# Performance work log

Hardware: AMD Instinct MI355X
Metric: run time of the kernel (lower is better)

The kernel has to match this reference:

```python
import jax, jax.numpy as jnp
import numpy as np

EPS = 1e-8  # torch CosineSimilarity default eps

def _normalize(x):
    # torch clamps each norm at eps before dividing
    n = jnp.sqrt(jnp.sum(x * x, axis=-1, keepdims=True))
    return x / jnp.maximum(n, EPS)

def _cross_entropy(logits, labels):
    logp = jax.nn.log_softmax(logits, axis=-1)
    return -jnp.mean(jnp.take_along_axis(logp, labels[:, None], axis=-1))

def setup_inputs() -> dict:
    key = jax.random.key(0)
    ks = jax.random.split(key, 7)
    B, M, D = 8192, 3129, 512
    return {
        'mm_proj': jax.random.normal(ks[0], (B, D), jnp.float32),
        'ans_embedding': jax.random.normal(ks[1], (M, D), jnp.float32),
        'v_max': jax.random.normal(ks[2], (B, D), jnp.float32),
        'mm': jax.random.normal(ks[3], (B, D), jnp.float32),
        'logits_q': jax.random.normal(ks[4], (B, M), jnp.float32),
        'logits_rubi': jax.random.normal(ks[5], (B, M), jnp.float32),
        'class_id': jax.random.randint(ks[6], (B, 1), 0, M, jnp.int64),
    }

def reference(mm_proj, ans_embedding, v_max, mm, logits_q, logits_rubi, class_id,
              question_loss_weight=1.0):
    cid = class_id.squeeze(1)  # [B]
    # NCE over cosine similarities: fuse normalize + GEMM instead of [B,M,D] expand
    g = _normalize(mm_proj)          # [B, D]
    a = _normalize(ans_embedding)    # [M, D]
    d_logit = jnp.einsum('bd,md->bm', g, a)  # [B, M] cosine matrix
    positive_dist = jnp.take_along_axis(d_logit, cid[:, None], axis=1)[:, 0]  # [B]
    num = jnp.exp(positive_dist)
    den = jnp.sum(jnp.exp(d_logit), axis=-1)
    loss_nce = jnp.mean(-jnp.log(num / den))
    # object cosine loss
    obj_dist = jnp.sum(_normalize(v_max) * _normalize(mm), axis=-1)  # [B]
    obj_loss = jnp.mean(1.0 - obj_dist)
    fusion_loss = (_cross_entropy(logits_rubi, cid) + obj_loss + loss_nce) / 3.0
    question_loss = _cross_entropy(logits_q, cid)
    loss = fusion_loss + question_loss_weight * question_loss
    # out['loss'], out['loss_mm_q'], out['loss_q']
    return jnp.stack([loss, fusion_loss, question_loss])
```

## Files before the change

kernel.cpp:

```cpp
#include <hip/hip_runtime.h>
#include <hip/hip_bf16.h>

#define B_N 8192
#define M_N 3129
#define M_PAD 3200
#define D_N 512

#define GLOBAL_AS __attribute__((address_space(1)))
#define LDS_AS __attribute__((address_space(3)))

typedef __bf16 bf16x8 __attribute__((ext_vector_type(8)));
typedef float f32x4 __attribute__((ext_vector_type(4)));

#define PREP_G_BLOCKS   (B_N / 4)
#define PREP_A_BLOCKS   (M_PAD / 4)
#define PREP_OBJ_BLOCKS (B_N / 4)

__device__ __forceinline__ void normalize_row(
    const float* __restrict__ x, __bf16* __restrict__ y,
    int row, int nrows_src, int lane) {
  bf16x8 out;
  if (row >= nrows_src) {
    for (int j = 0; j < 8; ++j) out[j] = (__bf16)0.0f;
    *(bf16x8*)(y + (size_t)row * D_N + lane * 8) = out;
    return;
  }
  const float4* xr = (const float4*)(x + (size_t)row * D_N);
  float4 v0 = xr[lane * 2], v1 = xr[lane * 2 + 1];
  float s = v0.x*v0.x + v0.y*v0.y + v0.z*v0.z + v0.w*v0.w
          + v1.x*v1.x + v1.y*v1.y + v1.z*v1.z + v1.w*v1.w;
  for (int o = 1; o < 64; o <<= 1) s += __shfl_xor(s, o);
  float rn = 1.0f / fmaxf(sqrtf(s), 1e-8f);
  float vals[8] = {v0.x, v0.y, v0.z, v0.w, v1.x, v1.y, v1.z, v1.w};
  for (int j = 0; j < 8; ++j) out[j] = (__bf16)(vals[j] * rn);
  *(bf16x8*)(y + (size_t)row * D_N + lane * 8) = out;
}

__global__ __launch_bounds__(256) void prep_kernel(
    const float* __restrict__ mm_proj, const float* __restrict__ ans_emb,
    const float* __restrict__ v_max, const float* __restrict__ mm,
    __bf16* __restrict__ g, __bf16* __restrict__ a,
    float* __restrict__ obj) {
  int blk = blockIdx.x;
  int wid = threadIdx.x >> 6, lane = threadIdx.x & 63;
  if (blk < PREP_G_BLOCKS) {
    normalize_row(mm_proj, g, blk * 4 + wid, B_N, lane);
  } else if (blk < PREP_G_BLOCKS + PREP_A_BLOCKS) {
    normalize_row(ans_emb, a, (blk - PREP_G_BLOCKS) * 4 + wid, M_N, lane);
  } else {
    int b = (blk - PREP_G_BLOCKS - PREP_A_BLOCKS) * 4 + wid;
    const float4* vr = (const float4*)(v_max + (size_t)b * D_N);
    const float4* mr = (const float4*)(mm + (size_t)b * D_N);
    float4 a0 = vr[lane * 2], a1 = vr[lane * 2 + 1];
    float4 b0 = mr[lane * 2], b1 = mr[lane * 2 + 1];
    float sv = a0.x*a0.x + a0.y*a0.y + a0.z*a0.z + a0.w*a0.w
             + a1.x*a1.x + a1.y*a1.y + a1.z*a1.z + a1.w*a1.w;
    float sm = b0.x*b0.x + b0.y*b0.y + b0.z*b0.z + b0.w*b0.w
             + b1.x*b1.x + b1.y*b1.y + b1.z*b1.z + b1.w*b1.w;
    float sd = a0.x*b0.x + a0.y*b0.y + a0.z*b0.z + a0.w*b0.w
             + a1.x*b1.x + a1.y*b1.y + a1.z*b1.z + a1.w*b1.w;
    for (int o = 1; o < 64; o <<= 1) {
      sv += __shfl_xor(sv, o);
      sm += __shfl_xor(sm, o);
      sd += __shfl_xor(sd, o);
    }
    if (lane == 0) {
      float dist = sd / (fmaxf(sqrtf(sv), 1e-8f) * fmaxf(sqrtf(sm), 1e-8f));
      obj[b] = 1.0f - dist;
    }
  }
}

__global__ __launch_bounds__(256) void pos_kernel(
    const __bf16* __restrict__ g, const __bf16* __restrict__ a,
    const int* __restrict__ cid, float* __restrict__ pos) {
  int wid = threadIdx.x >> 6, lane = threadIdx.x & 63;
  int b = blockIdx.x * 4 + wid;
  if (b >= B_N) return;
  int label = cid[b];
  bf16x8 gv = *(const bf16x8*)(g + (size_t)b * D_N + lane * 8);
  bf16x8 av = *(const bf16x8*)(a + (size_t)label * D_N + lane * 8);
  float s = 0.0f;
  for (int j = 0; j < 8; ++j) s += (float)gv[j] * (float)av[j];
  for (int o = 1; o < 64; o <<= 1) s += __shfl_xor(s, o);
  if (lane == 0) pos[b] = s;
}

__global__ __launch_bounds__(256) void nce_gemm_kernel(
    const __bf16* __restrict__ g, const __bf16* __restrict__ a,
    float* __restrict__ den) {
  __shared__ __bf16 As[128 * 32];
  __shared__ __bf16 Bs[128 * 32];
  const int t = threadIdx.x;
  const int brow0 = blockIdx.y * 128;
  const int mrow0 = blockIdx.x * 128;
  const int lane = t & 63;
  const int wid = t >> 6;
  const int wrow = wid >> 1;
  const int wcol = wid & 1;
  const int r = lane & 15;
  const int quad = lane >> 4;

  f32x4 acc[4][4];
  for (int i = 0; i < 4; ++i)
    for (int j = 0; j < 4; ++j)
      acc[i][j] = f32x4{0.f, 0.f, 0.f, 0.f};

  for (int k0 = 0; k0 < D_N; k0 += 32) {
    __syncthreads();
    for (int i = 0; i < 2; ++i) {
      int s = t + i * 256;
      int row = s >> 2;
      int kq = (s & 3) << 3;
      const __bf16* ga = g + (size_t)(brow0 + row) * D_N + (k0 + kq);
      __builtin_amdgcn_global_load_lds((const GLOBAL_AS void*)ga,
                                       (LDS_AS void*)(As + s * 8), 16, 0, 0);
      const __bf16* gb = a + (size_t)(mrow0 + row) * D_N + (k0 + kq);
      __builtin_amdgcn_global_load_lds((const GLOBAL_AS void*)gb,
                                       (LDS_AS void*)(Bs + s * 8), 16, 0, 0);
    }
    __syncthreads();
    bf16x8 af[4], bf[4];
    for (int i = 0; i < 4; ++i)
      af[i] = *(const bf16x8*)(As + (wrow * 64 + i * 16 + r) * 32 + quad * 8);
    for (int j = 0; j < 4; ++j)
      bf[j] = *(const bf16x8*)(Bs + (wcol * 64 + j * 16 + r) * 32 + quad * 8);
    for (int i = 0; i < 4; ++i)
      for (int j = 0; j < 4; ++j)
        acc[i][j] = __builtin_amdgcn_mfma_f32_16x16x32_bf16(af[i], bf[j],
                                                            acc[i][j], 0, 0, 0);
  }

  for (int i = 0; i < 4; ++i) {
    for (int reg = 0; reg < 4; ++reg) {
      float s = 0.0f;
      for (int j = 0; j < 4; ++j) {
        int m = mrow0 + wcol * 64 + j * 16 + r;
        if (m < M_N) s += __expf(acc[i][j][reg]);
      }
      s += __shfl_xor(s, 1);
      s += __shfl_xor(s, 2);
      s += __shfl_xor(s, 4);
      s += __shfl_xor(s, 8);
      if (r == 0) {
        int b = brow0 + wrow * 64 + i * 16 + quad * 4 + reg;
        atomicAdd(den + b, s);
      }
    }
  }
}

#define CE_CHUNKS 784

__global__ __launch_bounds__(256) void ce_kernel(
    const float* __restrict__ lq, const float* __restrict__ lr,
    const int* __restrict__ cid,
    float* __restrict__ ce_q, float* __restrict__ ce_r) {
  __shared__ float Lq[CE_CHUNKS * 4];
  __shared__ float Lr[CE_CHUNKS * 4];
  const int b = blockIdx.x;
  const int t = threadIdx.x;
  const size_t start = ((size_t)b * M_N) & ~(size_t)3;
  const int mis = b & 3;
  const size_t TOTAL = (size_t)B_N * M_N;

#pragma unroll
  for (int k = 0; k < 3; ++k) {
    int c = t + k * 256;
    size_t gi = start + (size_t)c * 4;
    if (gi + 4 > TOTAL) gi = TOTAL - 4;
    __builtin_amdgcn_global_load_lds((const GLOBAL_AS void*)(lq + gi),
                                     (LDS_AS void*)(Lq + c * 4), 16, 0, 0);
    __builtin_amdgcn_global_load_lds((const GLOBAL_AS void*)(lr + gi),
                                     (LDS_AS void*)(Lr + c * 4), 16, 0, 0);
  }
  if (t < CE_CHUNKS - 768) {
    int c = t + 768;
    size_t gi = start + (size_t)c * 4;
    if (gi + 4 > TOTAL) gi = TOTAL - 4;
    __builtin_amdgcn_global_load_lds((const GLOBAL_AS void*)(lq + gi),
                                     (LDS_AS void*)(Lq + c * 4), 16, 0, 0);
    __builtin_amdgcn_global_load_lds((const GLOBAL_AS void*)(lr + gi),
                                     (LDS_AS void*)(Lr + c * 4), 16, 0, 0);
  }
  __syncthreads();

  const int lo = mis, hi = mis + M_N;
  float sq = 0.0f, sr = 0.0f;
#pragma unroll
  for (int k = 0; k < 4; ++k) {
    int c = t + k * 256;
    if (c < CE_CHUNKS) {
      float4 q = *(const float4*)(Lq + c * 4);
      float4 p = *(const float4*)(Lr + c * 4);
      int e = c * 4;
      if (e + 0 >= lo && e + 0 < hi) { sq += __expf(q.x); sr += __expf(p.x); }
      if (e + 1 >= lo && e + 1 < hi) { sq += __expf(q.y); sr += __expf(p.y); }
      if (e + 2 >= lo && e + 2 < hi) { sq += __expf(q.z); sr += __expf(p.z); }
      if (e + 3 >= lo && e + 3 < hi) { sq += __expf(q.w); sr += __expf(p.w); }
    }
  }
  for (int o = 1; o < 64; o <<= 1) {
    sq += __shfl_xor(sq, o);
    sr += __shfl_xor(sr, o);
  }
  __shared__ float ssq[4], ssr[4];
  int wid = t >> 6;
  if ((t & 63) == 0) { ssq[wid] = sq; ssr[wid] = sr; }
  __syncthreads();
  if (t == 0) {
    float tq = ssq[0] + ssq[1] + ssq[2] + ssq[3];
    float tr = ssr[0] + ssr[1] + ssr[2] + ssr[3];
    int label = cid[b];
    ce_q[b] = logf(tq) - Lq[mis + label];
    ce_r[b] = logf(tr) - Lr[mis + label];
  }
}

__global__ __launch_bounds__(256) void final_reduce_kernel(
    const float* __restrict__ den, const float* __restrict__ pos,
    const float* __restrict__ ce_q, const float* __restrict__ ce_r,
    const float* __restrict__ obj, float* __restrict__ acc) {
  int b = blockIdx.x * 256 + threadIdx.x;
  float s_nce = logf(den[b]) - pos[b];
  float s_ceq = ce_q[b];
  float s_cer = ce_r[b];
  float s_obj = obj[b];
  for (int o = 1; o < 64; o <<= 1) {
    s_nce += __shfl_xor(s_nce, o);
    s_ceq += __shfl_xor(s_ceq, o);
    s_cer += __shfl_xor(s_cer, o);
    s_obj += __shfl_xor(s_obj, o);
  }
  __shared__ float red[4][4];
  int wid = threadIdx.x >> 6;
  if ((threadIdx.x & 63) == 0) {
    red[wid][0] = s_nce; red[wid][1] = s_ceq;
    red[wid][2] = s_cer; red[wid][3] = s_obj;
  }
  __syncthreads();
  if (threadIdx.x < 4) {
    float v = red[0][threadIdx.x] + red[1][threadIdx.x]
            + red[2][threadIdx.x] + red[3][threadIdx.x];
    atomicAdd(acc + threadIdx.x, v);
  }
}

__global__ void final_combine_kernel(const float* __restrict__ acc,
                                     float* __restrict__ out) {
  if (threadIdx.x == 0) {
    float nce = acc[0] / (float)B_N;
    float ceq = acc[1] / (float)B_N;
    float cer = acc[2] / (float)B_N;
    float ob  = acc[3] / (float)B_N;
    float fusion = (cer + ob + nce) * (1.0f / 3.0f);
    out[0] = fusion + ceq;
    out[1] = fusion;
    out[2] = ceq;
  }
}

extern "C" void kernel_launch(void* const* d_in, const int* in_sizes, int n_in,
                              void* d_out, int out_size, void* d_ws, size_t ws_size,
                              hipStream_t stream) {
  const float* mm_proj     = (const float*)d_in[0];
  const float* ans_emb     = (const float*)d_in[1];
  const float* v_max       = (const float*)d_in[2];
  const float* mm          = (const float*)d_in[3];
  const float* logits_q    = (const float*)d_in[4];
  const float* logits_rubi = (const float*)d_in[5];
  const int*   cid         = (const int*)d_in[6];
  float* out = (float*)d_out;

  char* ws = (char*)d_ws;
  __bf16* g = (__bf16*)ws;
  __bf16* a = (__bf16*)(ws + 8388608);
  float* den  = (float*)(ws + 8388608 + 3276800);
  float* acc  = den + B_N;
  float* pos  = acc + 4;
  float* ce_q = pos + B_N;
  float* ce_r = ce_q + B_N;
  float* obj  = ce_r + B_N;

  hipMemsetAsync(den, 0, (size_t)(B_N + 4) * sizeof(float), stream);

  prep_kernel<<<PREP_G_BLOCKS + PREP_A_BLOCKS + PREP_OBJ_BLOCKS, 256, 0,
                stream>>>(mm_proj, ans_emb, v_max, mm, g, a, obj);
  pos_kernel<<<B_N / 4, 256, 0, stream>>>(g, a, cid, pos);
  nce_gemm_kernel<<<dim3(M_PAD / 128, B_N / 128), 256, 0, stream>>>(g, a, den);
  ce_kernel<<<B_N, 256, 0, stream>>>(logits_q, logits_rubi, cid, ce_q, ce_r);
  final_reduce_kernel<<<B_N / 256, 256, 0, stream>>>(den, pos, ce_q, ce_r,
                                                     obj, acc);
  final_combine_kernel<<<1, 64, 0, stream>>>(acc, out);
}
```

Measured before the change: 325.1 us.

## Flatten cross-entropy row sums into grid-stride wave chunks with atomic row accumulation

Replaces the per-row CE kernel, which staged each 3129-float row into LDS, with a flat streaming kernel. Each wave reads contiguous 1 KB chunks of both logits arrays directly into registers, splits each chunk's exp-sum between at most two rows, and atomically adds into per-row sums. The label logit gather and the log move into the final reduce kernel. This aims for fully coalesced aligned loads and no LDS round-trip or block syncs, at the cost of many atomics and a longer memset.

```diff
diff --git a/kernel.cpp b/kernel.cpp
--- a/kernel.cpp
+++ b/kernel.cpp
@@ -5,6 +5,11 @@
 #define M_N 3129
 #define M_PAD 3200
 #define D_N 512
+
+#define CE_WPA 100128
+#define CE_WTOT (2 * CE_WPA)
+#define CE_WAVES 8344
+#define CE_BLOCKS 2086
 
 #define GLOBAL_AS __attribute__((address_space(1)))
 #define LDS_AS __attribute__((address_space(3)))
@@ -150,81 +155,66 @@
   }
 }
 
-#define CE_CHUNKS 784
-
-__global__ __launch_bounds__(256) void ce_kernel(
+__global__ __launch_bounds__(256) void ce_sum_kernel(
     const float* __restrict__ lq, const float* __restrict__ lr,
-    const int* __restrict__ cid,
-    float* __restrict__ ce_q, float* __restrict__ ce_r) {
-  __shared__ float Lq[CE_CHUNKS * 4];
-  __shared__ float Lr[CE_CHUNKS * 4];
-  const int b = blockIdx.x;
-  const int t = threadIdx.x;
-  const size_t start = ((size_t)b * M_N) & ~(size_t)3;
-  const int mis = b & 3;
-  const size_t TOTAL = (size_t)B_N * M_N;
-
+    float* __restrict__ rowsum) {
+  const int lane = threadIdx.x & 63;
+  const int gw = (int)((blockIdx.x * 256 + threadIdx.x) >> 6);
+#pragma unroll 1
+  for (int gidx = 0; gidx < 6; ++gidx) {
+    float4 v[4];
+    unsigned e0[4];
+    int arr[4];
 #pragma unroll
-  for (int k = 0; k < 3; ++k) {
-    int c = t + k * 256;
-    size_t gi = start + (size_t)c * 4;
-    if (gi + 4 > TOTAL) gi = TOTAL - 4;
-    __builtin_amdgcn_global_load_lds((const GLOBAL_AS void*)(lq + gi),
-                                     (LDS_AS void*)(Lq + c * 4), 16, 0, 0);
-    __builtin_amdgcn_global_load_lds((const GLOBAL_AS void*)(lr + gi),
-                                     (LDS_AS void*)(Lr + c * 4), 16, 0, 0);
-  }
-  if (t < CE_CHUNKS - 768) {
-    int c = t + 768;
-    size_t gi = start + (size_t)c * 4;
-    if (gi + 4 > TOTAL) gi = TOTAL - 4;
-    __builtin_amdgcn_global_load_lds((const GLOBAL_AS void*)(lq + gi),
-                                     (LDS_AS void*)(Lq + c * 4), 16, 0, 0);
-    __builtin_amdgcn_global_load_lds((const GLOBAL_AS void*)(lr + gi),
-                                     (LDS_AS void*)(Lr + c * 4), 16, 0, 0);
-  }
-  __syncthreads();
-
-  const int lo = mis, hi = mis + M_N;
-  float sq = 0.0f, sr = 0.0f;
+    for (int k = 0; k < 4; ++k) {
+      int w = gw + (gidx * 4 + k) * CE_WAVES;
+      int aidx = (w >= CE_WPA) ? 1 : 0;
+      unsigned chunk = (unsigned)(w - aidx * CE_WPA) * 64u + (unsigned)lane;
+      e0[k] = chunk * 4u;
+      arr[k] = aidx;
+      const float* base = aidx ? lr : lq;
+      v[k] = *(const float4*)(base + (size_t)chunk * 4u);
+    }
 #pragma unroll
-  for (int k = 0; k < 4; ++k) {
-    int c = t + k * 256;
-    if (c < CE_CHUNKS) {
-      float4 q = *(const float4*)(Lq + c * 4);
-      float4 p = *(const float4*)(Lr + c * 4);
-      int e = c * 4;
-      if (e + 0 >= lo && e + 0 < hi) { sq += __expf(q.x); sr += __expf(p.x); }
-      if (e + 1 >= lo && e + 1 < hi) { sq += __expf(q.y); sr += __expf(p.y); }
-      if (e + 2 >= lo && e + 2 < hi) { sq += __expf(q.z); sr += __expf(p.z); }
-      if (e + 3 >= lo && e + 3 < hi) { sq += __expf(q.w); sr += __expf(p.w); }
-    }
-  }
-  for (int o = 1; o < 64; o <<= 1) {
-    sq += __shfl_xor(sq, o);
-    sr += __shfl_xor(sr, o);
-  }
-  __shared__ float ssq[4], ssr[4];
-  int wid = t >> 6;
-  if ((t & 63) == 0) { ssq[wid] = sq; ssr[wid] = sr; }
-  __syncthreads();
-  if (t == 0) {
-    float tq = ssq[0] + ssq[1] + ssq[2] + ssq[3];
-    float tr = ssr[0] + ssr[1] + ssr[2] + ssr[3];
-    int label = cid[b];
-    ce_q[b] = logf(tq) - Lq[mis + label];
-    ce_r[b] = logf(tr) - Lr[mis + label];
+    for (int k = 0; k < 4; ++k) {
+      unsigned row0 = e0[k] / M_N;
+      unsigned bound = (row0 + 1u) * M_N;
+      float ex0 = __expf(v[k].x), ex1 = __expf(v[k].y),
+            ex2 = __expf(v[k].z), ex3 = __expf(v[k].w);
+      float s_lo = 0.f, s_hi = 0.f;
+      if (e0[k] + 0u < bound) s_lo += ex0; else s_hi += ex0;
+      if (e0[k] + 1u < bound) s_lo += ex1; else s_hi += ex1;
+      if (e0[k] + 2u < bound) s_lo += ex2; else s_hi += ex2;
+      if (e0[k] + 3u < bound) s_lo += ex3; else s_hi += ex3;
+      unsigned rA = (unsigned)__builtin_amdgcn_readfirstlane((int)row0);
+      float cA = (row0 == rA) ? s_lo : 0.f;
+      float cB = (row0 == rA) ? s_hi : s_lo;
+      for (int o = 1; o < 64; o <<= 1) {
+        cA += __shfl_xor(cA, o);
+        cB += __shfl_xor(cB, o);
+      }
+      if (lane == 0) {
+        float* rs = rowsum + (arr[k] ? B_N : 0);
+        atomicAdd(rs + rA, cA);
+        if (cB != 0.f) atomicAdd(rs + rA + 1, cB);
+      }
+    }
   }
 }
 
 __global__ __launch_bounds__(256) void final_reduce_kernel(
     const float* __restrict__ den, const float* __restrict__ pos,
-    const float* __restrict__ ce_q, const float* __restrict__ ce_r,
-    const float* __restrict__ obj, float* __restrict__ acc) {
+    const float* __restrict__ rowsum,
+    const float* __restrict__ lq, const float* __restrict__ lr,
+    const int* __restrict__ cid, const float* __restrict__ obj,
+    float* __restrict__ acc) {
   int b = blockIdx.x * 256 + threadIdx.x;
+  int lab = cid[b];
+  float xq = lq[(size_t)b * M_N + lab];
+  float xr = lr[(size_t)b * M_N + lab];
   float s_nce = logf(den[b]) - pos[b];
-  float s_ceq = ce_q[b];
-  float s_cer = ce_r[b];
+  float s_ceq = logf(rowsum[b]) - xq;
+  float s_cer = logf(rowsum[B_N + b]) - xr;
   float s_obj = obj[b];
   for (int o = 1; o < 64; o <<= 1) {
     s_nce += __shfl_xor(s_nce, o);
@@ -275,21 +265,21 @@
   char* ws = (char*)d_ws;
   __bf16* g = (__bf16*)ws;
   __bf16* a = (__bf16*)(ws + 8388608);
-  float* den  = (float*)(ws + 8388608 + 3276800);
-  float* acc  = den + B_N;
-  float* pos  = acc + 4;
-  float* ce_q = pos + B_N;
-  float* ce_r = ce_q + B_N;
-  float* obj  = ce_r + B_N;
-
-  hipMemsetAsync(den, 0, (size_t)(B_N + 4) * sizeof(float), stream);
+  float* den    = (float*)(ws + 8388608 + 3276800);
+  float* rowsum = den + B_N;
+  float* acc    = rowsum + 2 * B_N;
+  float* pos    = acc + 4;
+  float* obj    = pos + B_N;
+
+  hipMemsetAsync(den, 0, (size_t)(3 * B_N + 4) * sizeof(float), stream);
 
   prep_kernel<<<PREP_G_BLOCKS + PREP_A_BLOCKS + PREP_OBJ_BLOCKS, 256, 0,
                 stream>>>(mm_proj, ans_emb, v_max, mm, g, a, obj);
   pos_kernel<<<B_N / 4, 256, 0, stream>>>(g, a, cid, pos);
   nce_gemm_kernel<<<dim3(M_PAD / 128, B_N / 128), 256, 0, stream>>>(g, a, den);
-  ce_kernel<<<B_N, 256, 0, stream>>>(logits_q, logits_rubi, cid, ce_q, ce_r);
-  final_reduce_kernel<<<B_N / 256, 256, 0, stream>>>(den, pos, ce_q, ce_r,
-                                                     obj, acc);
+  ce_sum_kernel<<<CE_BLOCKS, 256, 0, stream>>>(logits_q, logits_rubi, rowsum);
+  final_reduce_kernel<<<B_N / 256, 256, 0, stream>>>(den, pos, rowsum,
+                                                     logits_q, logits_rubi,
+                                                     cid, obj, acc);
   final_combine_kernel<<<1, 64, 0, stream>>>(acc, out);
 }
```

Measured after the change: 338.4 us. 1.04x slower.
